# Optimization experiments

Hardware: AMD Instinct MI355X
Metric: run time of the kernel (lower is better)

## Reference

```python
import jax, jax.numpy as jnp
import numpy as np


def setup_inputs() -> dict:
    key = jax.random.key(0)
    k_x, k_w, k_s, k_b = jax.random.split(key, 4)
    B, S, D_IN, D_OUT = 8, 2048, 4096, 4096
    x = jax.random.normal(k_x, (B, S, D_IN), dtype=jnp.float32)
    # int8-valued weights stored as int32 (values in [-128, 127])
    quantized_weights = jax.random.randint(k_w, (D_OUT, D_IN), -128, 128, dtype=jnp.int32)
    scales = jax.random.normal(k_s, (D_OUT,), dtype=jnp.float32)
    bias = jax.random.normal(k_b, (D_OUT,), dtype=jnp.float32)
    return {"x": x, "quantized_weights": quantized_weights, "scales": scales, "bias": bias}


def reference(x, quantized_weights, scales, bias):
    # Per-output-channel dequant: W[o, i] = q[o, i] * scales[o]
    dequantized_weight = quantized_weights.astype(x.dtype) * scales[:, None].astype(x.dtype)
    # F.linear: y = x @ W^T + b
    return jnp.einsum('bsi,oi->bso', x, dequantized_weight) + bias.astype(x.dtype)
```

## Files before the change

### kernel.cpp

```cpp
#include <hip/hip_runtime.h>

#define M_DIM 16384
#define N_DIM 4096
#define K_DIM 4096
#define NTOT 128

typedef __attribute__((ext_vector_type(4))) float f32x4;
typedef __attribute__((ext_vector_type(8))) short bf16x8;
typedef __attribute__((ext_vector_type(4))) int   i32x4;

__device__ __forceinline__ short f2bf(float f) {
    unsigned int u = __builtin_bit_cast(unsigned int, f);
    u += 0x7FFFu + ((u >> 16) & 1u);
    return (short)(u >> 16);
}

__global__ __launch_bounds__(256)
void quant_kernel(const float* __restrict__ x, const int* __restrict__ q,
                  char* __restrict__ x8, char* __restrict__ w8,
                  float* __restrict__ rs) {
    const int tid = threadIdx.x;
    if (blockIdx.x < M_DIM) {
        const int row = blockIdx.x;
        const float* xr = x + (size_t)row * K_DIM;
        f32x4 v[4];
        float am = 0.f;
#pragma unroll
        for (int p = 0; p < 4; ++p) {
            v[p] = *(const f32x4*)(xr + p * 1024 + tid * 4);
#pragma unroll
            for (int e = 0; e < 4; ++e) am = fmaxf(am, fabsf(v[p][e]));
        }
#pragma unroll
        for (int off = 32; off >= 1; off >>= 1)
            am = fmaxf(am, __shfl_xor(am, off, 64));
        __shared__ float smax[4];
        if ((tid & 63) == 0) smax[tid >> 6] = am;
        __syncthreads();
        am = fmaxf(fmaxf(smax[0], smax[1]), fmaxf(smax[2], smax[3]));
        const float inv = am > 0.f ? 127.f / am : 0.f;
        if (tid == 0) rs[row] = am / 127.f;
        int* o32 = (int*)(x8 + (size_t)row * K_DIM);
#pragma unroll
        for (int p = 0; p < 4; ++p) {
            const int b0 = (int)rintf(v[p][0] * inv);
            const int b1 = (int)rintf(v[p][1] * inv);
            const int b2 = (int)rintf(v[p][2] * inv);
            const int b3 = (int)rintf(v[p][3] * inv);
            o32[p * 256 + tid] = (b0 & 255) | ((b1 & 255) << 8) | ((b2 & 255) << 16) | ((b3 & 255) << 24);
        }
    } else {
        const long n = (long)N_DIM * K_DIM;
        long i = ((long)(blockIdx.x - M_DIM) * 256 + tid) * 16;
        const long stride = 2048L * 256 * 16;
        for (; i < n; i += stride) {
            i32x4 o;
#pragma unroll
            for (int j = 0; j < 4; ++j) {
                i32x4 a = *(const i32x4*)(q + i + j * 4);
                o[j] = (a[0] & 255) | ((a[1] & 255) << 8) | ((a[2] & 255) << 16) | ((a[3] & 255) << 24);
            }
            *(i32x4*)(w8 + i) = o;
        }
    }
}

__device__ __forceinline__ void load_lds16(const void* g, void* l) {
    __builtin_amdgcn_global_load_lds((const __attribute__((address_space(1))) void*)g,
                                     (__attribute__((address_space(3))) void*)l, 16, 0, 0);
}

#define BAR() __builtin_amdgcn_s_barrier()
#define VM(n) asm volatile("s_waitcnt vmcnt(" #n ")" ::: "memory")
#define SETP1 __builtin_amdgcn_s_setprio(1)
#define SETP0 __builtin_amdgcn_s_setprio(0)

__global__ __launch_bounds__(512, 2)
void gemm_persist(const char* __restrict__ A, const char* __restrict__ Bw,
                  const float* __restrict__ rs, const float* __restrict__ scales,
                  const float* __restrict__ bias, float* __restrict__ out) {
    __shared__ char lds[2][4][128 * 128];

    const int tid  = threadIdx.x;
    const int lane = tid & 63;
    const int w    = tid >> 6;
    const int wm   = w >> 2;
    const int wn   = w & 3;
    const int lrow = lane & 15;
    const int lkg  = lane >> 4;
    const int sx   = lane & 7;

    const int swz = ((int)blockIdx.x & 7) * 32 + ((int)blockIdx.x >> 3);
    const int bn  = (swz & 15) * 256;
    const int bm0 = (swz >> 4) * 256;

    const char* aS[2];
    const char* bS[2];
#pragma unroll
    for (int L = 0; L < 2; ++L) {
        const int c   = L * 512 + tid;
        const int row = c >> 3;
        const int kc  = (c & 7) ^ (row & 7);
        const int mA  = bm0 + ((row >> 6) << 7) + (row & 63);
        const int nB  = bn  + ((row >> 5) << 6) + (row & 31);
        aS[L] = A  + (size_t)mA * K_DIM + kc * 16;
        bS[L] = Bw + (size_t)nB * K_DIM + kc * 16;
    }
    const int wofs = w << 10;

#define KO_A(g, q) ((long)((g) >> 5) * (4096L * K_DIM) + (long)((g) & 31) * 128 + (long)(q) * (64L * K_DIM))
#define KO_B(g, nh) ((long)((g) & 31) * 128 + (long)(nh) * (32L * K_DIM))

#define STAGE_A(buf, q, g) do { \
    char* d = &lds[buf][q][wofs]; \
    const long ko = KO_A(g, q); \
    load_lds16(aS[0] + ko, d); \
    load_lds16(aS[1] + ko, d + 8192); \
} while (0)

#define STAGE_B(buf, nh, g) do { \
    char* d = &lds[buf][2 + (nh)][wofs]; \
    const long ko = KO_B(g, nh); \
    load_lds16(bS[0] + ko, d); \
    load_lds16(bS[1] + ko, d + 8192); \
} while (0)

    const int aoff = (wm << 6) + lrow;
    const int boff = (wn << 5) + lrow;

#define RD_A(buf, q, sub, ks) \
    (*(const i32x4*)&lds[buf][q][((aoff + (sub) * 16) << 7) + (((((ks) << 2) + lkg) ^ sx) << 4)])
#define RD_B(buf, nh, sub, ks) \
    (*(const i32x4*)&lds[buf][2 + (nh)][((boff + (sub) * 16) << 7) + (((((ks) << 2) + lkg) ^ sx) << 4)])

    i32x4 acc[8][4];
#pragma unroll
    for (int i = 0; i < 8; ++i)
#pragma unroll
        for (int j = 0; j < 4; ++j)
            acc[i][j] = (i32x4){0, 0, 0, 0};

    i32x4 aF[4][2], bF0[2][2], bF1[2][2];

#define LOAD_AF(buf, q) do { \
    _Pragma("unroll") for (int ii = 0; ii < 4; ++ii) { \
        aF[ii][0] = RD_A(buf, q, ii, 0); aF[ii][1] = RD_A(buf, q, ii, 1); } \
} while (0)
#define LOAD_BF(dst, buf, nh) do { \
    _Pragma("unroll") for (int jj = 0; jj < 2; ++jj) { \
        dst[jj][0] = RD_B(buf, nh, jj, 0); dst[jj][1] = RD_B(buf, nh, jj, 1); } \
} while (0)
#define MMA_Q(mh, nh, BREG) do { \
    _Pragma("unroll") for (int ii = 0; ii < 4; ++ii) \
    _Pragma("unroll") for (int jj = 0; jj < 2; ++jj) \
    _Pragma("unroll") for (int ks = 0; ks < 2; ++ks) \
        acc[(mh) * 4 + ii][(nh) * 2 + jj] = __builtin_amdgcn_mfma_i32_16x16x64_i8( \
            aF[ii][ks], BREG[jj][ks], acc[(mh) * 4 + ii][(nh) * 2 + jj], 0, 0, 0); \
} while (0)

    STAGE_A(0, 0, 0); STAGE_B(0, 0, 0); STAGE_B(0, 1, 0); STAGE_A(0, 1, 0);
    STAGE_A(1, 0, 1); STAGE_B(1, 0, 1); STAGE_B(1, 1, 1);

    for (int g = 0; g < NTOT; ++g) {
        const int buf = g & 1;

        if (g + 1 < NTOT) STAGE_A(buf ^ 1, 1, g + 1);
        if (g == NTOT - 1) { VM(2); } else { VM(10); }
        BAR();
        SETP1;
        LOAD_AF(buf, 0);
        LOAD_BF(bF0, buf, 0);
        MMA_Q(0, 0, bF0);
        LOAD_BF(bF1, buf, 1);
        MMA_Q(0, 1, bF1);
        SETP0;
        BAR();

        if (g + 2 < NTOT) {
            STAGE_A(buf, 0, g + 2); STAGE_B(buf, 0, g + 2); STAGE_B(buf, 1, g + 2);
        }
        if (g == NTOT - 1) { VM(0); } else if (g == NTOT - 2) { VM(8); } else { VM(14); }
        BAR();
        SETP1;
        LOAD_AF(buf, 1);
        MMA_Q(1, 0, bF0);
        MMA_Q(1, 1, bF1);
        SETP0;
        BAR();

        if ((g & 31) == 31) {
            const int bm = bm0 + (g >> 5) * 4096;
#pragma unroll
            for (int i = 0; i < 8; ++i) {
                const int r0 = bm + (wm << 7) + i * 16 + (lkg << 2);
                const f32x4 rsv = *(const f32x4*)&rs[r0];
#pragma unroll
                for (int j = 0; j < 4; ++j) {
                    const int col = bn + (wn << 6) + j * 16 + lrow;
                    const float sc = scales[col];
                    const float bb = bias[col];
#pragma unroll
                    for (int r = 0; r < 4; ++r)
                        out[(size_t)(r0 + r) * N_DIM + col] = (float)acc[i][j][r] * (rsv[r] * sc) + bb;
                    acc[i][j] = (i32x4){0, 0, 0, 0};
                }
            }
        }
    }
#undef KO_A
#undef KO_B
#undef STAGE_A
#undef STAGE_B
#undef RD_A
#undef RD_B
#undef LOAD_AF
#undef LOAD_BF
#undef MMA_Q
}

__global__ __launch_bounds__(256)
void gemm_fallback(const float* __restrict__ Xf, const int* __restrict__ Qw,
                   const float* __restrict__ scales, const float* __restrict__ bias,
                   float* __restrict__ out) {
    __shared__ short a_lds[128 * 64];
    __shared__ short b_lds[128 * 64];
    const int tid  = threadIdx.x;
    const int lane = tid & 63;
    const int wid  = tid >> 6;
    const int wm   = wid >> 1;
    const int wn   = wid & 1;
    const int bn = (blockIdx.x % (N_DIM / 128)) * 128;
    const int bm = (blockIdx.x / (N_DIM / 128)) * 128;
    const int lrow = lane & 15;
    const int lkg  = lane >> 4;

    f32x4 acc[4][4];
#pragma unroll
    for (int i = 0; i < 4; ++i)
#pragma unroll
        for (int j = 0; j < 4; ++j)
            acc[i][j] = (f32x4){0.f, 0.f, 0.f, 0.f};

    for (int k0 = 0; k0 < K_DIM; k0 += 64) {
#pragma unroll
        for (int t = 0; t < 4; ++t) {
            const int ch  = t * 256 + tid;
            const int row = ch >> 3;
            const int kc  = (ch & 7) ^ (row & 7);
            {
                const float* sa = Xf + (size_t)(bm + row) * K_DIM + k0 + kc * 8;
                f32x4 a0 = *(const f32x4*)sa;
                f32x4 a1 = *(const f32x4*)(sa + 4);
                bf16x8 r;
                r[0] = f2bf(a0[0]); r[1] = f2bf(a0[1]); r[2] = f2bf(a0[2]); r[3] = f2bf(a0[3]);
                r[4] = f2bf(a1[0]); r[5] = f2bf(a1[1]); r[6] = f2bf(a1[2]); r[7] = f2bf(a1[3]);
                *(bf16x8*)&a_lds[ch * 8] = r;
            }
            {
                const int* sb = Qw + (size_t)(bn + row) * K_DIM + k0 + kc * 8;
                i32x4 q0 = *(const i32x4*)sb;
                i32x4 q1 = *(const i32x4*)(sb + 4);
                bf16x8 r;
                r[0] = f2bf((float)q0[0]); r[1] = f2bf((float)q0[1]);
                r[2] = f2bf((float)q0[2]); r[3] = f2bf((float)q0[3]);
                r[4] = f2bf((float)q1[0]); r[5] = f2bf((float)q1[1]);
                r[6] = f2bf((float)q1[2]); r[7] = f2bf((float)q1[3]);
                *(bf16x8*)&b_lds[ch * 8] = r;
            }
        }
        __syncthreads();
#pragma unroll
        for (int ks = 0; ks < 2; ++ks) {
            const int kgl = ks * 4 + lkg;
            bf16x8 af[4], bfr[4];
#pragma unroll
            for (int i = 0; i < 4; ++i) {
                const int am = wm * 64 + i * 16 + lrow;
                af[i]  = *(const bf16x8*)&a_lds[am * 64 + ((kgl ^ (am & 7)) << 3)];
                const int bnn = wn * 64 + i * 16 + lrow;
                bfr[i] = *(const bf16x8*)&b_lds[bnn * 64 + ((kgl ^ (bnn & 7)) << 3)];
            }
#pragma unroll
            for (int i = 0; i < 4; ++i)
#pragma unroll
                for (int j = 0; j < 4; ++j)
                    acc[i][j] = __builtin_amdgcn_mfma_f32_16x16x32_bf16(af[i], bfr[j], acc[i][j], 0, 0, 0);
        }
        __syncthreads();
    }
#pragma unroll
    for (int j = 0; j < 4; ++j) {
        const int col = bn + wn * 64 + j * 16 + lrow;
        const float s  = scales[col];
        const float bb = bias[col];
#pragma unroll
        for (int i = 0; i < 4; ++i) {
            const int row0 = bm + wm * 64 + i * 16 + lkg * 4;
#pragma unroll
            for (int r = 0; r < 4; ++r)
                out[(size_t)(row0 + r) * N_DIM + col] = acc[i][j][r] * s + bb;
        }
    }
}

extern "C" void kernel_launch(void* const* d_in, const int* in_sizes, int n_in,
                              void* d_out, int out_size, void* d_ws, size_t ws_size,
                              hipStream_t stream) {
    const float* x      = (const float*)d_in[0];
    const int*   qw     = (const int*)d_in[1];
    const float* scales = (const float*)d_in[2];
    const float* bias   = (const float*)d_in[3];
    float* out = (float*)d_out;

    const size_t x_elems = (size_t)M_DIM * K_DIM;
    const size_t w_elems = (size_t)N_DIM * K_DIM;
    const size_t need    = x_elems + w_elems + M_DIM * sizeof(float);

    if (ws_size >= need) {
        char*  x8 = (char*)d_ws;
        char*  w8 = x8 + x_elems;
        float* rs = (float*)(w8 + w_elems);
        quant_kernel<<<M_DIM + 2048, 256, 0, stream>>>(x, qw, x8, w8, rs);
        gemm_persist<<<256, 512, 0, stream>>>(x8, w8, rs, scales, bias, out);
    } else {
        const dim3 grid((M_DIM / 128) * (N_DIM / 128));
        gemm_fallback<<<grid, 256, 0, stream>>>(x, qw, scales, bias, out);
    }
}
```

Measured before the change: 361.2 us.

## Replace persistent 256x256 int8 GEMM with non-persistent 128x128 tiled kernel

Swaps the persistent 512-thread kernel, whose blocks each loop over four M tiles of 256x256, for a conventional grid of 4096 blocks of 256 threads that each compute one 128x128 output tile. The K loop now splits each step into four quarter MMAs, with finer-grained staging of the next K tile between them. The aim is better load balance and latency hiding, trading away data reuse per block. Smaller tiles mean more global and LDS traffic per FLOP, and many more block launches.

```diff
diff --git a/kernel.cpp b/kernel.cpp
--- a/kernel.cpp
+++ b/kernel.cpp
@@ -3,7 +3,7 @@
 #define M_DIM 16384
 #define N_DIM 4096
 #define K_DIM 4096
-#define NTOT 128
+#define NT 32
 
 typedef __attribute__((ext_vector_type(4))) float f32x4;
 typedef __attribute__((ext_vector_type(8))) short bf16x8;
@@ -75,147 +75,125 @@
 #define SETP1 __builtin_amdgcn_s_setprio(1)
 #define SETP0 __builtin_amdgcn_s_setprio(0)
 
-__global__ __launch_bounds__(512, 2)
-void gemm_persist(const char* __restrict__ A, const char* __restrict__ Bw,
-                  const float* __restrict__ rs, const float* __restrict__ scales,
-                  const float* __restrict__ bias, float* __restrict__ out) {
-    __shared__ char lds[2][4][128 * 128];
+__global__ __launch_bounds__(256, 2)
+void gemm2b_i8(const char* __restrict__ A, const char* __restrict__ Bw,
+               const float* __restrict__ rs, const float* __restrict__ scales,
+               const float* __restrict__ bias, float* __restrict__ out) {
+    __shared__ char lds[2][2][128 * 128];
 
     const int tid  = threadIdx.x;
     const int lane = tid & 63;
     const int w    = tid >> 6;
-    const int wm   = w >> 2;
-    const int wn   = w & 3;
+    const int wm   = w >> 1;
+    const int wn   = w & 1;
     const int lrow = lane & 15;
     const int lkg  = lane >> 4;
     const int sx   = lane & 7;
 
-    const int swz = ((int)blockIdx.x & 7) * 32 + ((int)blockIdx.x >> 3);
-    const int bn  = (swz & 15) * 256;
-    const int bm0 = (swz >> 4) * 256;
-
-    const char* aS[2];
-    const char* bS[2];
-#pragma unroll
-    for (int L = 0; L < 2; ++L) {
-        const int c   = L * 512 + tid;
-        const int row = c >> 3;
-        const int kc  = (c & 7) ^ (row & 7);
-        const int mA  = bm0 + ((row >> 6) << 7) + (row & 63);
-        const int nB  = bn  + ((row >> 5) << 6) + (row & 31);
-        aS[L] = A  + (size_t)mA * K_DIM + kc * 16;
-        bS[L] = Bw + (size_t)nB * K_DIM + kc * 16;
-    }
-    const int wofs = w << 10;
-
-#define KO_A(g, q) ((long)((g) >> 5) * (4096L * K_DIM) + (long)((g) & 31) * 128 + (long)(q) * (64L * K_DIM))
-#define KO_B(g, nh) ((long)((g) & 31) * 128 + (long)(nh) * (32L * K_DIM))
-
-#define STAGE_A(buf, q, g) do { \
-    char* d = &lds[buf][q][wofs]; \
-    const long ko = KO_A(g, q); \
-    load_lds16(aS[0] + ko, d); \
-    load_lds16(aS[1] + ko, d + 8192); \
+    const int nwg = gridDim.x;
+    const int swz = ((int)blockIdx.x & 7) * (nwg >> 3) + ((int)blockIdx.x >> 3);
+    const int bn  = (swz & 31) << 7;
+    const int bm  = (swz >> 5) << 7;
+
+    long gOff[2][2];
+#pragma unroll
+    for (int h = 0; h < 2; ++h)
+#pragma unroll
+        for (int L = 0; L < 2; ++L) {
+            const int c   = h * 256 + L * 512 + tid;
+            const int row = c >> 3;
+            const int kc  = (c & 7) ^ (row & 7);
+            gOff[h][L] = (long)row * K_DIM + kc * 16;
+        }
+    const char* aB = A  + (size_t)bm * K_DIM;
+    const char* bB = Bw + (size_t)bn * K_DIM;
+
+#define STAGE(reg, buf, h, kt) do { \
+    const char* gb = (reg) ? bB : aB; \
+    load_lds16(gb + gOff[h][0] + (long)(kt) * 128, \
+               &lds[buf][reg][((h) << 12) + (w << 10)]); \
+    load_lds16(gb + gOff[h][1] + (long)(kt) * 128, \
+               &lds[buf][reg][((h) << 12) + 8192 + (w << 10)]); \
 } while (0)
 
-#define STAGE_B(buf, nh, g) do { \
-    char* d = &lds[buf][2 + (nh)][wofs]; \
-    const long ko = KO_B(g, nh); \
-    load_lds16(bS[0] + ko, d); \
-    load_lds16(bS[1] + ko, d + 8192); \
-} while (0)
-
-    const int aoff = (wm << 6) + lrow;
-    const int boff = (wn << 5) + lrow;
-
-#define RD_A(buf, q, sub, ks) \
-    (*(const i32x4*)&lds[buf][q][((aoff + (sub) * 16) << 7) + (((((ks) << 2) + lkg) ^ sx) << 4)])
-#define RD_B(buf, nh, sub, ks) \
-    (*(const i32x4*)&lds[buf][2 + (nh)][((boff + (sub) * 16) << 7) + (((((ks) << 2) + lkg) ^ sx) << 4)])
-
-    i32x4 acc[8][4];
-#pragma unroll
-    for (int i = 0; i < 8; ++i)
+#define RD_A(buf, sub, ks) \
+    (*(const i32x4*)&lds[buf][0][(((wm << 6) + (sub) * 16 + lrow) << 7) + (((((ks) << 2) + lkg) ^ sx) << 4)])
+#define RD_B(buf, jj, ks) \
+    (*(const i32x4*)&lds[buf][1][(((wn << 6) + (jj) * 16 + lrow) << 7) + (((((ks) << 2) + lkg) ^ sx) << 4)])
+
+    i32x4 acc[4][4];
+#pragma unroll
+    for (int i = 0; i < 4; ++i)
 #pragma unroll
         for (int j = 0; j < 4; ++j)
             acc[i][j] = (i32x4){0, 0, 0, 0};
 
-    i32x4 aF[4][2], bF0[2][2], bF1[2][2];
-
-#define LOAD_AF(buf, q) do { \
-    _Pragma("unroll") for (int ii = 0; ii < 4; ++ii) { \
-        aF[ii][0] = RD_A(buf, q, ii, 0); aF[ii][1] = RD_A(buf, q, ii, 1); } \
+    i32x4 aFa[2][2], aFb[2][2], bFa[2][2], bFb[2][2];
+
+#define MMA4(I0, J0, AF, BF) do { \
+    SETP1; \
+    _Pragma("unroll") for (int s = 0; s < 2; ++s) \
+    _Pragma("unroll") for (int j = 0; j < 2; ++j) \
+    _Pragma("unroll") for (int k = 0; k < 2; ++k) \
+        acc[(I0) + s][(J0) + j] = __builtin_amdgcn_mfma_i32_16x16x64_i8( \
+            AF[s][k], BF[j][k], acc[(I0) + s][(J0) + j], 0, 0, 0); \
+    SETP0; \
 } while (0)
-#define LOAD_BF(dst, buf, nh) do { \
-    _Pragma("unroll") for (int jj = 0; jj < 2; ++jj) { \
-        dst[jj][0] = RD_B(buf, nh, jj, 0); dst[jj][1] = RD_B(buf, nh, jj, 1); } \
-} while (0)
-#define MMA_Q(mh, nh, BREG) do { \
-    _Pragma("unroll") for (int ii = 0; ii < 4; ++ii) \
-    _Pragma("unroll") for (int jj = 0; jj < 2; ++jj) \
-    _Pragma("unroll") for (int ks = 0; ks < 2; ++ks) \
-        acc[(mh) * 4 + ii][(nh) * 2 + jj] = __builtin_amdgcn_mfma_i32_16x16x64_i8( \
-            aF[ii][ks], BREG[jj][ks], acc[(mh) * 4 + ii][(nh) * 2 + jj], 0, 0, 0); \
-} while (0)
-
-    STAGE_A(0, 0, 0); STAGE_B(0, 0, 0); STAGE_B(0, 1, 0); STAGE_A(0, 1, 0);
-    STAGE_A(1, 0, 1); STAGE_B(1, 0, 1); STAGE_B(1, 1, 1);
-
-    for (int g = 0; g < NTOT; ++g) {
-        const int buf = g & 1;
-
-        if (g + 1 < NTOT) STAGE_A(buf ^ 1, 1, g + 1);
-        if (g == NTOT - 1) { VM(2); } else { VM(10); }
-        BAR();
-        SETP1;
-        LOAD_AF(buf, 0);
-        LOAD_BF(bF0, buf, 0);
-        MMA_Q(0, 0, bF0);
-        LOAD_BF(bF1, buf, 1);
-        MMA_Q(0, 1, bF1);
-        SETP0;
-        BAR();
-
-        if (g + 2 < NTOT) {
-            STAGE_A(buf, 0, g + 2); STAGE_B(buf, 0, g + 2); STAGE_B(buf, 1, g + 2);
-        }
-        if (g == NTOT - 1) { VM(0); } else if (g == NTOT - 2) { VM(8); } else { VM(14); }
-        BAR();
-        SETP1;
-        LOAD_AF(buf, 1);
-        MMA_Q(1, 0, bF0);
-        MMA_Q(1, 1, bF1);
-        SETP0;
-        BAR();
-
-        if ((g & 31) == 31) {
-            const int bm = bm0 + (g >> 5) * 4096;
-#pragma unroll
-            for (int i = 0; i < 8; ++i) {
-                const int r0 = bm + (wm << 7) + i * 16 + (lkg << 2);
-                const f32x4 rsv = *(const f32x4*)&rs[r0];
-#pragma unroll
-                for (int j = 0; j < 4; ++j) {
-                    const int col = bn + (wn << 6) + j * 16 + lrow;
-                    const float sc = scales[col];
-                    const float bb = bias[col];
-#pragma unroll
-                    for (int r = 0; r < 4; ++r)
-                        out[(size_t)(r0 + r) * N_DIM + col] = (float)acc[i][j][r] * (rsv[r] * sc) + bb;
-                    acc[i][j] = (i32x4){0, 0, 0, 0};
-                }
-            }
-        }
-    }
-#undef KO_A
-#undef KO_B
-#undef STAGE_A
-#undef STAGE_B
+
+    STAGE(1, 0, 0, 0); STAGE(0, 0, 0, 0); STAGE(1, 0, 1, 0); STAGE(0, 0, 1, 0);
+    VM(4);
+    BAR();
+
+    for (int t = 0; t < NT; ++t) {
+        const int buf = t & 1, nb = buf ^ 1;
+        const bool st = (t + 1 < NT);
+
+#pragma unroll
+        for (int k = 0; k < 2; ++k) {
+            aFa[0][k] = RD_A(buf, 0, k); aFa[1][k] = RD_A(buf, 1, k);
+            bFa[0][k] = RD_B(buf, 0, k); bFa[1][k] = RD_B(buf, 1, k);
+        }
+        if (st) STAGE(1, nb, 0, t + 1);
+        if (st) { VM(4); } else { VM(2); }
+        BAR(); MMA4(0, 0, aFa, bFa); BAR();
+
+#pragma unroll
+        for (int k = 0; k < 2; ++k) {
+            bFb[0][k] = RD_B(buf, 2, k); bFb[1][k] = RD_B(buf, 3, k);
+        }
+        if (st) STAGE(0, nb, 0, t + 1);
+        if (st) { VM(4); } else { VM(0); }
+        BAR(); MMA4(0, 2, aFa, bFb); BAR();
+
+#pragma unroll
+        for (int k = 0; k < 2; ++k) {
+            aFb[0][k] = RD_A(buf, 2, k); aFb[1][k] = RD_A(buf, 3, k);
+        }
+        if (st) { STAGE(1, nb, 1, t + 1); VM(4); }
+        BAR(); MMA4(2, 0, aFb, bFa); BAR();
+
+        if (st) { STAGE(0, nb, 1, t + 1); VM(4); }
+        BAR(); MMA4(2, 2, aFb, bFb); BAR();
+    }
+
+#pragma unroll
+    for (int i = 0; i < 4; ++i) {
+        const int r0 = bm + (wm << 6) + i * 16 + (lkg << 2);
+        const f32x4 rsv = *(const f32x4*)&rs[r0];
+#pragma unroll
+        for (int j = 0; j < 4; ++j) {
+            const int col = bn + (wn << 6) + j * 16 + lrow;
+            const float sc = scales[col];
+            const float bb = bias[col];
+#pragma unroll
+            for (int r = 0; r < 4; ++r)
+                out[(size_t)(r0 + r) * N_DIM + col] = (float)acc[i][j][r] * (rsv[r] * sc) + bb;
+        }
+    }
+#undef STAGE
 #undef RD_A
 #undef RD_B
-#undef LOAD_AF
-#undef LOAD_BF
-#undef MMA_Q
+#undef MMA4
 }
 
 __global__ __launch_bounds__(256)
@@ -321,7 +299,8 @@
         char*  w8 = x8 + x_elems;
         float* rs = (float*)(w8 + w_elems);
         quant_kernel<<<M_DIM + 2048, 256, 0, stream>>>(x, qw, x8, w8, rs);
-        gemm_persist<<<256, 512, 0, stream>>>(x8, w8, rs, scales, bias, out);
+        const dim3 grid((M_DIM / 128) * (N_DIM / 128));
+        gemm2b_i8<<<grid, 256, 0, stream>>>(x8, w8, rs, scales, bias, out);
     } else {
         const dim3 grid((M_DIM / 128) * (N_DIM / 128));
         gemm_fallback<<<grid, 256, 0, stream>>>(x, qw, scales, bias, out);
```

Result: slower. 466.1 us (median of 2 runs) (+29.0%).
